# Kernel optimization log

Measured on AMD Instinct MI355X. Metric: run time of the kernel, lower is better.

Reference implementation:

```python
import jax, jax.numpy as jnp
import numpy as np

NUM_GRAPHS = 16
NODES_PER_GRAPH = 2048
FEAT_DIM = 512


def setup_inputs() -> dict:
    key = jax.random.key(0)
    batched_h = jax.random.normal(key, (NUM_GRAPHS * NODES_PER_GRAPH, FEAT_DIM), dtype=jnp.float32)
    return {
        "batched_h": batched_h,
        "num_graphs": NUM_GRAPHS,
        "nodes_per_graph": NODES_PER_GRAPH,
    }


def reference(batched_h, num_graphs, nodes_per_graph):
    # Wq = Wk = Identity (module defaults), return_feat = False.
    # Per graph g: sm[i, j] = sum_d (q[i, d] - k[j, d])^2
    # computed via the Gram-matrix identity ||q||^2 + ||k||^2 - 2 q k^T,
    # which replaces the original O(n^2 * d) tiled intermediate with a GEMM.
    h = batched_h.reshape(num_graphs, nodes_per_graph, -1)  # [G, N, D]
    q = h
    k = h
    sq_q = jnp.sum(q * q, axis=-1)                      # [G, N]
    sq_k = jnp.sum(k * k, axis=-1)                      # [G, N]
    gram = jnp.einsum("gnd,gmd->gnm", q, k)             # [G, N, N]
    sm = sq_q[:, :, None] + sq_k[:, None, :] - 2.0 * gram
    return sm  # [G, N, N] stacked analogue of the per-graph inst_out list
```

## Files before the change

kernel.cpp:

```cpp
#include <hip/hip_runtime.h>
#include <hip/hip_bf16.h>
#include <stdint.h>

#define NG 16
#define NN 2048
#define DD 512
#define NROW (NG * NN)
#define NTILE 16
#define NPAIR 136
#define NXCD 8

typedef __attribute__((ext_vector_type(8))) short short8;
typedef __attribute__((ext_vector_type(4))) float f32x4;

__device__ inline unsigned short f2bf(float f) {
  union { float f; unsigned int u; } c;
  c.f = f;
  unsigned int x = c.u;
  unsigned int r = (x + 0x7fffu + ((x >> 16) & 1u)) >> 16;
  return (unsigned short)r;
}

__device__ inline void gload_lds16(const void* g, void* l) {
  __builtin_amdgcn_global_load_lds(
      (const __attribute__((address_space(1))) void*)g,
      (__attribute__((address_space(3))) void*)l, 16, 0, 0);
}

template <bool WRITE_BF>
__global__ __launch_bounds__(256) void prep_kernel(const float* __restrict__ h,
                                                   unsigned short* __restrict__ hbf,
                                                   float* __restrict__ sq) {
  const int row = blockIdx.x * 4 + (threadIdx.x >> 6);
  const int lane = threadIdx.x & 63;
  const float* hr = h + (size_t)row * DD;
  float4 v0 = ((const float4*)hr)[lane * 2];
  float4 v1 = ((const float4*)hr)[lane * 2 + 1];
  float s = v0.x * v0.x + v0.y * v0.y + v0.z * v0.z + v0.w * v0.w +
            v1.x * v1.x + v1.y * v1.y + v1.z * v1.z + v1.w * v1.w;
  if (WRITE_BF) {
    union { unsigned short us[8]; uint4 u4; } pk;
    pk.us[0] = f2bf(v0.x); pk.us[1] = f2bf(v0.y);
    pk.us[2] = f2bf(v0.z); pk.us[3] = f2bf(v0.w);
    pk.us[4] = f2bf(v1.x); pk.us[5] = f2bf(v1.y);
    pk.us[6] = f2bf(v1.z); pk.us[7] = f2bf(v1.w);
    ((uint4*)(hbf + (size_t)row * DD))[lane] = pk.u4;
  }
#pragma unroll
  for (int off = 32; off > 0; off >>= 1) s += __shfl_xor(s, off, 64);
  if (lane == 0) sq[row] = s;
}

template <bool USE_WS>
__global__ __launch_bounds__(256) void gram_kernel(const unsigned short* __restrict__ hbf,
                                                   const float* __restrict__ hf,
                                                   const float* __restrict__ sq,
                                                   float* __restrict__ out) {
  __shared__ __align__(16) unsigned short As[128 * 64];
  __shared__ __align__(16) unsigned short Bs[128 * 64];

  const int t = threadIdx.x;
  const int lane = t & 63, wid = t >> 6;
  const int wr = wid >> 1, wc = wid & 1;
  const int l16 = lane & 15, lhi = lane >> 4;

  const int bid = blockIdx.x;
  const int xcd = bid & (NXCD - 1);
  const int slot = bid >> 3;
  const int half = (slot >= NPAIR) ? 1 : 0;
  const int g = xcd * 2 + half;
  int p = slot - half * NPAIR;
  int bi = 0, rowlen = NTILE;
  while (p >= rowlen) { p -= rowlen; ++bi; --rowlen; }
  const int bj = bi + p;

  const size_t rowA = (size_t)g * NN + bi * 128;
  const size_t rowB = (size_t)g * NN + bj * 128;

  f32x4 acc[4][4];
#pragma unroll
  for (int m = 0; m < 4; ++m)
#pragma unroll
    for (int n = 0; n < 4; ++n) acc[m][n] = (f32x4){0.f, 0.f, 0.f, 0.f};

  for (int kt = 0; kt < DD / 64; ++kt) {
    if (USE_WS) {
      const char* Ab = (const char*)(hbf + rowA * DD + kt * 64);
      const char* Bb = (const char*)(hbf + rowB * DD + kt * 64);
#pragma unroll
      for (int r = 0; r < 4; ++r) {
        const int off = r * 4096 + t * 16;
        const int rw = off >> 7;
        const int cb = off & 127;
        gload_lds16(Ab + (size_t)rw * (DD * 2) + cb, (char*)As + r * 4096 + wid * 1024);
        gload_lds16(Bb + (size_t)rw * (DD * 2) + cb, (char*)Bs + r * 4096 + wid * 1024);
      }
    } else {
      const float* Af = hf + rowA * DD + kt * 64;
      const float* Bf = hf + rowB * DD + kt * 64;
#pragma unroll
      for (int r = 0; r < 4; ++r) {
        const int off = r * 4096 + t * 16;
        const int rw = off >> 7;
        const int c0 = (off & 127) >> 1;
        float4 a0 = *(const float4*)(Af + (size_t)rw * DD + c0);
        float4 a1 = *(const float4*)(Af + (size_t)rw * DD + c0 + 4);
        float4 b0 = *(const float4*)(Bf + (size_t)rw * DD + c0);
        float4 b1 = *(const float4*)(Bf + (size_t)rw * DD + c0 + 4);
        union { unsigned short us[8]; uint4 u4; } pa, pb;
        pa.us[0] = f2bf(a0.x); pa.us[1] = f2bf(a0.y);
        pa.us[2] = f2bf(a0.z); pa.us[3] = f2bf(a0.w);
        pa.us[4] = f2bf(a1.x); pa.us[5] = f2bf(a1.y);
        pa.us[6] = f2bf(a1.z); pa.us[7] = f2bf(a1.w);
        pb.us[0] = f2bf(b0.x); pb.us[1] = f2bf(b0.y);
        pb.us[2] = f2bf(b0.z); pb.us[3] = f2bf(b0.w);
        pb.us[4] = f2bf(b1.x); pb.us[5] = f2bf(b1.y);
        pb.us[6] = f2bf(b1.z); pb.us[7] = f2bf(b1.w);
        *(uint4*)((char*)As + off) = pa.u4;
        *(uint4*)((char*)Bs + off) = pb.u4;
      }
    }
    __syncthreads();
#pragma unroll
    for (int kk = 0; kk < 2; ++kk) {
      short8 af[4], bfr[4];
#pragma unroll
      for (int m = 0; m < 4; ++m)
        af[m] = *(const short8*)&As[(wr * 64 + m * 16 + l16) * 64 + kk * 32 + lhi * 8];
#pragma unroll
      for (int n = 0; n < 4; ++n)
        bfr[n] = *(const short8*)&Bs[(wc * 64 + n * 16 + l16) * 64 + kk * 32 + lhi * 8];
#pragma unroll
      for (int m = 0; m < 4; ++m)
#pragma unroll
        for (int n = 0; n < 4; ++n)
          acc[m][n] = __builtin_amdgcn_mfma_f32_16x16x32_bf16(af[m], bfr[n], acc[m][n], 0, 0, 0);
    }
    __syncthreads();
  }

  float sqr[4][4];
  float sqc[4];
#pragma unroll
  for (int m = 0; m < 4; ++m)
#pragma unroll
    for (int r = 0; r < 4; ++r)
      sqr[m][r] = sq[rowA + wr * 64 + m * 16 + lhi * 4 + r];
#pragma unroll
  for (int n = 0; n < 4; ++n) sqc[n] = sq[rowB + wc * 64 + n * 16 + l16];

  float* outg = out + (size_t)g * NN * NN;
  const int I = bi * 128 + wr * 64;
  const int J = bj * 128 + wc * 64;
  const bool offdiag = (bi != bj);

#pragma unroll
  for (int m = 0; m < 4; ++m)
#pragma unroll
    for (int n = 0; n < 4; ++n) {
      f32x4 v;
      v.x = sqr[m][0] + sqc[n] - 2.0f * acc[m][n][0];
      v.y = sqr[m][1] + sqc[n] - 2.0f * acc[m][n][1];
      v.z = sqr[m][2] + sqc[n] - 2.0f * acc[m][n][2];
      v.w = sqr[m][3] + sqc[n] - 2.0f * acc[m][n][3];
      __builtin_nontemporal_store(
          v, (f32x4*)&outg[(size_t)(J + n * 16 + l16) * NN + I + m * 16 + lhi * 4]);
      if (offdiag) {
        const int jn = J + n * 16 + l16;
        const int i0 = I + m * 16 + lhi * 4;
        __builtin_nontemporal_store(v.x, &outg[(size_t)(i0 + 0) * NN + jn]);
        __builtin_nontemporal_store(v.y, &outg[(size_t)(i0 + 1) * NN + jn]);
        __builtin_nontemporal_store(v.z, &outg[(size_t)(i0 + 2) * NN + jn]);
        __builtin_nontemporal_store(v.w, &outg[(size_t)(i0 + 3) * NN + jn]);
      }
    }
}

extern "C" void kernel_launch(void* const* d_in, const int* in_sizes, int n_in,
                              void* d_out, int out_size, void* d_ws, size_t ws_size,
                              hipStream_t stream) {
  const float* h = (const float*)d_in[0];
  float* out = (float*)d_out;

  float* sq = (float*)d_ws;
  unsigned short* hbf = (unsigned short*)((char*)d_ws + NROW * 4);
  const size_t need_ws = (size_t)NROW * 4 + (size_t)NROW * DD * 2;
  const bool use_ws = ws_size >= need_ws;

  if (use_ws) {
    prep_kernel<true><<<NROW / 4, 256, 0, stream>>>(h, hbf, sq);
    gram_kernel<true><<<NG * NPAIR, 256, 0, stream>>>(hbf, nullptr, sq, out);
  } else {
    prep_kernel<false><<<NROW / 4, 256, 0, stream>>>(h, nullptr, sq);
    gram_kernel<false><<<NG * NPAIR, 256, 0, stream>>>(nullptr, h, sq, out);
  }
}
```

Before: 126.1 us.

## Load MFMA operands directly from global memory, dropping LDS staging and barriers

The gram kernel no longer stages A and B tiles through shared memory with global_load_lds and __syncthreads. Each lane now loads its MFMA fragments straight from global memory (bf16 workspace or fp32 with inline conversion), with the K loop fully unrolled so the compiler can hoist loads and overlap them with MFMAs. The epilogue loop order is also swapped (n outer, m inner). The aim is to remove barrier and LDS round-trip cost, in exchange for more global and L2 traffic, since operands are no longer shared across waves, and for uncoalesced 16-byte row-strided loads.

```diff
diff --git a/kernel.cpp b/kernel.cpp
--- a/kernel.cpp
+++ b/kernel.cpp
@@ -19,12 +19,6 @@
   unsigned int x = c.u;
   unsigned int r = (x + 0x7fffu + ((x >> 16) & 1u)) >> 16;
   return (unsigned short)r;
-}
-
-__device__ inline void gload_lds16(const void* g, void* l) {
-  __builtin_amdgcn_global_load_lds(
-      (const __attribute__((address_space(1))) void*)g,
-      (__attribute__((address_space(3))) void*)l, 16, 0, 0);
 }
 
 template <bool WRITE_BF>
@@ -56,9 +50,6 @@
                                                    const float* __restrict__ hf,
                                                    const float* __restrict__ sq,
                                                    float* __restrict__ out) {
-  __shared__ __align__(16) unsigned short As[128 * 64];
-  __shared__ __align__(16) unsigned short Bs[128 * 64];
-
   const int t = threadIdx.x;
   const int lane = t & 63, wid = t >> 6;
   const int wr = wid >> 1, wc = wid & 1;
@@ -83,60 +74,78 @@
 #pragma unroll
     for (int n = 0; n < 4; ++n) acc[m][n] = (f32x4){0.f, 0.f, 0.f, 0.f};
 
-  for (int kt = 0; kt < DD / 64; ++kt) {
-    if (USE_WS) {
-      const char* Ab = (const char*)(hbf + rowA * DD + kt * 64);
-      const char* Bb = (const char*)(hbf + rowB * DD + kt * 64);
-#pragma unroll
-      for (int r = 0; r < 4; ++r) {
-        const int off = r * 4096 + t * 16;
-        const int rw = off >> 7;
-        const int cb = off & 127;
-        gload_lds16(Ab + (size_t)rw * (DD * 2) + cb, (char*)As + r * 4096 + wid * 1024);
-        gload_lds16(Bb + (size_t)rw * (DD * 2) + cb, (char*)Bs + r * 4096 + wid * 1024);
-      }
-    } else {
-      const float* Af = hf + rowA * DD + kt * 64;
-      const float* Bf = hf + rowB * DD + kt * 64;
-#pragma unroll
-      for (int r = 0; r < 4; ++r) {
-        const int off = r * 4096 + t * 16;
-        const int rw = off >> 7;
-        const int c0 = (off & 127) >> 1;
-        float4 a0 = *(const float4*)(Af + (size_t)rw * DD + c0);
-        float4 a1 = *(const float4*)(Af + (size_t)rw * DD + c0 + 4);
-        float4 b0 = *(const float4*)(Bf + (size_t)rw * DD + c0);
-        float4 b1 = *(const float4*)(Bf + (size_t)rw * DD + c0 + 4);
-        union { unsigned short us[8]; uint4 u4; } pa, pb;
-        pa.us[0] = f2bf(a0.x); pa.us[1] = f2bf(a0.y);
-        pa.us[2] = f2bf(a0.z); pa.us[3] = f2bf(a0.w);
-        pa.us[4] = f2bf(a1.x); pa.us[5] = f2bf(a1.y);
-        pa.us[6] = f2bf(a1.z); pa.us[7] = f2bf(a1.w);
-        pb.us[0] = f2bf(b0.x); pb.us[1] = f2bf(b0.y);
-        pb.us[2] = f2bf(b0.z); pb.us[3] = f2bf(b0.w);
-        pb.us[4] = f2bf(b1.x); pb.us[5] = f2bf(b1.y);
-        pb.us[6] = f2bf(b1.z); pb.us[7] = f2bf(b1.w);
-        *(uint4*)((char*)As + off) = pa.u4;
-        *(uint4*)((char*)Bs + off) = pb.u4;
+  if (USE_WS) {
+    const unsigned short* Arow[4];
+    const unsigned short* Brow[4];
+#pragma unroll
+    for (int m = 0; m < 4; ++m)
+      Arow[m] = hbf + (rowA + wr * 64 + m * 16 + l16) * DD + lhi * 8;
+#pragma unroll
+    for (int n = 0; n < 4; ++n)
+      Brow[n] = hbf + (rowB + wc * 64 + n * 16 + l16) * DD + lhi * 8;
+
+#pragma unroll
+    for (int kt = 0; kt < DD / 64; ++kt) {
+#pragma unroll
+      for (int kk = 0; kk < 2; ++kk) {
+        const int ko = kt * 64 + kk * 32;
+        short8 af[4], bfr[4];
+#pragma unroll
+        for (int m = 0; m < 4; ++m) af[m] = *(const short8*)(Arow[m] + ko);
+#pragma unroll
+        for (int n = 0; n < 4; ++n) bfr[n] = *(const short8*)(Brow[n] + ko);
+#pragma unroll
+        for (int m = 0; m < 4; ++m)
+#pragma unroll
+          for (int n = 0; n < 4; ++n)
+            acc[m][n] = __builtin_amdgcn_mfma_f32_16x16x32_bf16(af[m], bfr[n], acc[m][n], 0, 0, 0);
       }
     }
-    __syncthreads();
-#pragma unroll
-    for (int kk = 0; kk < 2; ++kk) {
-      short8 af[4], bfr[4];
-#pragma unroll
-      for (int m = 0; m < 4; ++m)
-        af[m] = *(const short8*)&As[(wr * 64 + m * 16 + l16) * 64 + kk * 32 + lhi * 8];
-#pragma unroll
-      for (int n = 0; n < 4; ++n)
-        bfr[n] = *(const short8*)&Bs[(wc * 64 + n * 16 + l16) * 64 + kk * 32 + lhi * 8];
-#pragma unroll
-      for (int m = 0; m < 4; ++m)
-#pragma unroll
-        for (int n = 0; n < 4; ++n)
-          acc[m][n] = __builtin_amdgcn_mfma_f32_16x16x32_bf16(af[m], bfr[n], acc[m][n], 0, 0, 0);
+  } else {
+    const float* Arow[4];
+    const float* Brow[4];
+#pragma unroll
+    for (int m = 0; m < 4; ++m)
+      Arow[m] = hf + (rowA + wr * 64 + m * 16 + l16) * DD + lhi * 8;
+#pragma unroll
+    for (int n = 0; n < 4; ++n)
+      Brow[n] = hf + (rowB + wc * 64 + n * 16 + l16) * DD + lhi * 8;
+
+#pragma unroll
+    for (int kt = 0; kt < DD / 64; ++kt) {
+#pragma unroll
+      for (int kk = 0; kk < 2; ++kk) {
+        const int ko = kt * 64 + kk * 32;
+        short8 af[4], bfr[4];
+#pragma unroll
+        for (int m = 0; m < 4; ++m) {
+          float4 lo = *(const float4*)(Arow[m] + ko);
+          float4 hi = *(const float4*)(Arow[m] + ko + 4);
+          union { unsigned short us[8]; short8 s8; } pk;
+          pk.us[0] = f2bf(lo.x); pk.us[1] = f2bf(lo.y);
+          pk.us[2] = f2bf(lo.z); pk.us[3] = f2bf(lo.w);
+          pk.us[4] = f2bf(hi.x); pk.us[5] = f2bf(hi.y);
+          pk.us[6] = f2bf(hi.z); pk.us[7] = f2bf(hi.w);
+          af[m] = pk.s8;
+        }
+#pragma unroll
+        for (int n = 0; n < 4; ++n) {
+          float4 lo = *(const float4*)(Brow[n] + ko);
+          float4 hi = *(const float4*)(Brow[n] + ko + 4);
+          union { unsigned short us[8]; short8 s8; } pk;
+          pk.us[0] = f2bf(lo.x); pk.us[1] = f2bf(lo.y);
+          pk.us[2] = f2bf(lo.z); pk.us[3] = f2bf(lo.w);
+          pk.us[4] = f2bf(hi.x); pk.us[5] = f2bf(hi.y);
+          pk.us[6] = f2bf(hi.z); pk.us[7] = f2bf(hi.w);
+          bfr[n] = pk.s8;
+        }
+#pragma unroll
+        for (int m = 0; m < 4; ++m)
+#pragma unroll
+          for (int n = 0; n < 4; ++n)
+            acc[m][n] = __builtin_amdgcn_mfma_f32_16x16x32_bf16(af[m], bfr[n], acc[m][n], 0, 0, 0);
+      }
     }
-    __syncthreads();
   }
 
   float sqr[4][4];
@@ -155,9 +164,9 @@
   const bool offdiag = (bi != bj);
 
 #pragma unroll
-  for (int m = 0; m < 4; ++m)
-#pragma unroll
-    for (int n = 0; n < 4; ++n) {
+  for (int n = 0; n < 4; ++n)
+#pragma unroll
+    for (int m = 0; m < 4; ++m) {
       f32x4 v;
       v.x = sqr[m][0] + sqc[n] - 2.0f * acc[m][n][0];
       v.y = sqr[m][1] + sqc[n] - 2.0f * acc[m][n][1];
```

After: 176.1 us. 1.4x slower.

## Stage gram epilogue through swizzled LDS for coalesced transposed and direct stores

Applied to the files above, without the earlier changes.

The epilogue now writes each half of the 128x128 output tile into an XOR-swizzled shared-memory buffer, reusing the A/B tile storage, then reads it back so both the direct block and the mirrored off-diagonal block are written with coalesced 16-byte rows. Before, the mirrored block was written with scattered 4-byte stores. The change targets write-coalescing inefficiency in the output-bound store phase, at the cost of extra LDS traffic and two more block-wide barriers.

```diff
diff --git a/kernel.cpp b/kernel.cpp
--- a/kernel.cpp
+++ b/kernel.cpp
@@ -56,8 +56,9 @@
                                                    const float* __restrict__ hf,
                                                    const float* __restrict__ sq,
                                                    float* __restrict__ out) {
-  __shared__ __align__(16) unsigned short As[128 * 64];
-  __shared__ __align__(16) unsigned short Bs[128 * 64];
+  __shared__ __align__(16) char smem[32768];
+  unsigned short* As = (unsigned short*)smem;
+  unsigned short* Bs = (unsigned short*)(smem + 16384);
 
   const int t = threadIdx.x;
   const int lane = t & 63, wid = t >> 6;
@@ -67,9 +68,9 @@
   const int bid = blockIdx.x;
   const int xcd = bid & (NXCD - 1);
   const int slot = bid >> 3;
-  const int half = (slot >= NPAIR) ? 1 : 0;
-  const int g = xcd * 2 + half;
-  int p = slot - half * NPAIR;
+  const int gh = (slot >= NPAIR) ? 1 : 0;
+  const int g = xcd * 2 + gh;
+  int p = slot - gh * NPAIR;
   int bi = 0, rowlen = NTILE;
   while (p >= rowlen) { p -= rowlen; ++bi; --rowlen; }
   const int bj = bi + p;
@@ -150,30 +151,57 @@
   for (int n = 0; n < 4; ++n) sqc[n] = sq[rowB + wc * 64 + n * 16 + l16];
 
   float* outg = out + (size_t)g * NN * NN;
-  const int I = bi * 128 + wr * 64;
-  const int J = bj * 128 + wc * 64;
   const bool offdiag = (bi != bj);
 
 #pragma unroll
-  for (int m = 0; m < 4; ++m)
-#pragma unroll
-    for (int n = 0; n < 4; ++n) {
-      f32x4 v;
-      v.x = sqr[m][0] + sqc[n] - 2.0f * acc[m][n][0];
-      v.y = sqr[m][1] + sqc[n] - 2.0f * acc[m][n][1];
-      v.z = sqr[m][2] + sqc[n] - 2.0f * acc[m][n][2];
-      v.w = sqr[m][3] + sqc[n] - 2.0f * acc[m][n][3];
-      __builtin_nontemporal_store(
-          v, (f32x4*)&outg[(size_t)(J + n * 16 + l16) * NN + I + m * 16 + lhi * 4]);
-      if (offdiag) {
-        const int jn = J + n * 16 + l16;
-        const int i0 = I + m * 16 + lhi * 4;
-        __builtin_nontemporal_store(v.x, &outg[(size_t)(i0 + 0) * NN + jn]);
-        __builtin_nontemporal_store(v.y, &outg[(size_t)(i0 + 1) * NN + jn]);
-        __builtin_nontemporal_store(v.z, &outg[(size_t)(i0 + 2) * NN + jn]);
-        __builtin_nontemporal_store(v.w, &outg[(size_t)(i0 + 3) * NN + jn]);
-      }
-    }
+  for (int hf = 0; hf < 2; ++hf) {
+    if (wc == hf) {
+#pragma unroll
+      for (int n = 0; n < 4; ++n)
+#pragma unroll
+        for (int m = 0; m < 4; ++m) {
+          f32x4 v;
+          v.x = sqr[m][0] + sqc[n] - 2.0f * acc[m][n][0];
+          v.y = sqr[m][1] + sqc[n] - 2.0f * acc[m][n][1];
+          v.z = sqr[m][2] + sqc[n] - 2.0f * acc[m][n][2];
+          v.w = sqr[m][3] + sqc[n] - 2.0f * acc[m][n][3];
+          const int jl = n * 16 + l16;
+          const int sw = (wr * 16 + m * 4 + lhi) ^ (jl & 31);
+          *(f32x4*)(smem + jl * 512 + (sw << 4)) = v;
+        }
+    }
+    __syncthreads();
+
+    {
+      const int jrow0 = bj * 128 + hf * 64;
+      const int s = t & 31;
+#pragma unroll
+      for (int k = 0; k < 8; ++k) {
+        const int jl = k * 8 + (t >> 5);
+        f32x4 v = *(const f32x4*)(smem + jl * 512 + ((s ^ (jl & 31)) << 4));
+        __builtin_nontemporal_store(
+            v, (f32x4*)&outg[(size_t)(jrow0 + jl) * NN + bi * 128 + s * 4]);
+      }
+    }
+    if (offdiag) {
+      const int jcol0 = bj * 128 + hf * 64;
+      const int j0 = (t & 15) * 4;
+#pragma unroll
+      for (int k = 0; k < 8; ++k) {
+        const int ip = k * 16 + (t >> 4);
+        f32x4 v;
+#pragma unroll
+        for (int d = 0; d < 4; ++d) {
+          const int jl = j0 + d;
+          v[d] = *(const float*)(smem + jl * 512 + ((((ip >> 2) ^ (jl & 31)) << 4)) +
+                                 (ip & 3) * 4);
+        }
+        __builtin_nontemporal_store(
+            v, (f32x4*)&outg[(size_t)(bi * 128 + ip) * NN + jcol0 + j0]);
+      }
+    }
+    if (hf == 0) __syncthreads();
+  }
 }
 
 extern "C" void kernel_launch(void* const* d_in, const int* in_sizes, int n_in,
```

After: 110.2 us. 12.6% less time.
